# Performance work log

Hardware: AMD Instinct MI355X
Metric: run time of the kernel (lower is better)

The kernel has to match this reference:

```python
import jax, jax.numpy as jnp
import numpy as np
import math

SUB = 0.8  # subset fraction (init kwarg)


def _capsule_weighted_average(x):
    # x: [B, I, O, D, H, W]; norm-weighted average over input caps (dim 1)
    n = jnp.linalg.norm(x, axis=3, keepdims=True)  # [B, I, O, 1, H, W]
    return (n * x).sum(axis=1) / n.sum(axis=1)      # [B, O, D, H, W]


def setup_inputs() -> dict:
    key = jax.random.key(0)
    # [B, input_caps, output_caps, pose_dim, H, W, kh, kw]
    x = jax.random.normal(key, (8, 32, 32, 8, 14, 14, 3, 3), dtype=jnp.float32)
    return {"x": x}


def reference(x):
    B, I, O, D, H, W = x.shape[:6]
    x = x.reshape(B, I, O, D, H, W, -1)             # flatten kernel positions -> K
    # norm-weighted average over the K kernel positions
    xn = jnp.linalg.norm(x, axis=3, keepdims=True)  # [B, I, O, 1, H, W, K]
    x = (xn * x).sum(axis=-1) / xn.sum(axis=-1)     # [B, I, O, D, H, W]

    v = _capsule_weighted_average(x)                # [B, O, D, H, W]

    # 'mse' metric: negative dot product between consensus v and each input capsule
    losses = -(v[:, None] * x).sum(axis=3)          # [B, I, O, H, W]
    subset_size = math.ceil(SUB * I)
    # kthvalue (k-th smallest) along input-caps dim
    thr = jnp.sort(losses, axis=1)[:, subset_size - 1:subset_size]  # [B, 1, O, H, W]
    choose = (losses <= thr).astype(x.dtype)[:, :, :, None]          # [B, I, O, 1, H, W]
    x = x * jax.lax.stop_gradient(choose)

    return _capsule_weighted_average(x)             # [B, O, D, H, W]
```

## Files before the change

kernel.cpp:

```cpp
#include <hip/hip_runtime.h>

#define B 8
#define I 32
#define O 32
#define D 8
#define H 14
#define W 14
#define K 9
#define WK (W*K)
#define DSTRIDE (H*W*K)
#define OSTRIDE (D*H*W*K)
#define ISTRIDE (O*D*H*W*K)
#define BSTRIDE ((size_t)I*ISTRIDE)
#define SUBSET 26

__global__ __launch_bounds__(256) void caps_route_kernel(const float* __restrict__ x,
                                                         float* __restrict__ out) {
    const int bid = blockIdx.x;
    const int h = bid % H;
    const int o = (bid / H) % O;
    const int b = bid / (H * O);
    const int t = threadIdx.x;

    __shared__ float xs[2][D][WK];
    __shared__ float nk[2][WK];
    __shared__ float ys[I][D][W];
    __shared__ float ns[I][W];
    __shared__ float ls[I][W];
    __shared__ float vsh[D][W];
    __shared__ float thr[W];

    const float* xb = x + (size_t)b * BSTRIDE + (size_t)o * OSTRIDE + (size_t)h * WK;

    for (int i0 = 0; i0 < I; i0 += 2) {
        const float2* src0 = (const float2*)(xb + (size_t)(i0    ) * ISTRIDE);
        const float2* src1 = (const float2*)(xb + (size_t)(i0 + 1) * ISTRIDE);
        #pragma unroll
        for (int it = 0; it < 4; ++it) {
            int f = t + it * 256;
            if (f < 1008) {
                int ii = f / 504;
                int r  = f - ii * 504;
                int d  = r / 63;
                int j  = r - d * 63;
                const float2* src = ii ? src1 : src0;
                float2 v2 = src[d * (DSTRIDE/2) + j];
                xs[ii][d][2*j]   = v2.x;
                xs[ii][d][2*j+1] = v2.y;
            }
        }
        __syncthreads();

        if (t < 2 * WK) {
            int ii = t / WK, j = t - (t / WK) * WK;
            float s = 0.f;
            #pragma unroll
            for (int d = 0; d < D; ++d) { float v = xs[ii][d][j]; s += v * v; }
            nk[ii][j] = sqrtf(s);
        }
        __syncthreads();

        if (t < 2 * D * W) {
            int ii = t / (D * W);
            int r  = t - ii * (D * W);
            int d  = r / W, w = r - (r / W) * W;
            float num = 0.f, den = 0.f;
            #pragma unroll
            for (int k = 0; k < K; ++k) {
                float nv = nk[ii][w * K + k];
                num += nv * xs[ii][d][w * K + k];
                den += nv;
            }
            ys[i0 + ii][d][w] = num / den;
        }
        __syncthreads();
    }

    for (int f = t; f < I * W; f += 256) {
        int i = f / W, w = f - (f / W) * W;
        float s = 0.f;
        #pragma unroll
        for (int d = 0; d < D; ++d) { float v = ys[i][d][w]; s += v * v; }
        ns[i][w] = sqrtf(s);
    }
    __syncthreads();

    if (t < D * W) {
        int d = t / W, w = t - (t / W) * W;
        float num = 0.f, den = 0.f;
        #pragma unroll
        for (int i = 0; i < I; ++i) {
            float nv = ns[i][w];
            num += nv * ys[i][d][w];
            den += nv;
        }
        vsh[d][w] = num / den;
    }
    __syncthreads();

    for (int f = t; f < I * W; f += 256) {
        int i = f / W, w = f - (f / W) * W;
        float s = 0.f;
        #pragma unroll
        for (int d = 0; d < D; ++d) s += vsh[d][w] * ys[i][d][w];
        ls[i][w] = -s;
    }
    __syncthreads();

    for (int f = t; f < I * W; f += 256) {
        int i = f / W, w = f - (f / W) * W;
        float li = ls[i][w];
        int rank = 0;
        #pragma unroll
        for (int j = 0; j < I; ++j) {
            float lj = ls[j][w];
            rank += (lj < li || (lj == li && j < i)) ? 1 : 0;
        }
        if (rank == SUBSET - 1) thr[w] = li;
    }
    __syncthreads();

    if (t < D * W) {
        int d = t / W, w = t - (t / W) * W;
        float tw = thr[w];
        float num = 0.f, den = 0.f;
        #pragma unroll
        for (int i = 0; i < I; ++i) {
            float m  = (ls[i][w] <= tw) ? 1.f : 0.f;
            float nv = m * ns[i][w];
            num += nv * ys[i][d][w];
            den += nv;
        }
        out[(((size_t)b * O + o) * D + d) * (H * W) + h * W + w] = num / den;
    }
}

extern "C" void kernel_launch(void* const* d_in, const int* in_sizes, int n_in,
                              void* d_out, int out_size, void* d_ws, size_t ws_size,
                              hipStream_t stream) {
    const float* x = (const float*)d_in[0];
    float* out = (float*)d_out;
    dim3 grid(B * O * H);
    dim3 block(256);
    caps_route_kernel<<<grid, block, 0, stream>>>(x, out);
}
```

Measured before the change: 619.2 us.

## Assign one thread per input-capsule and width position with register-resident loads

Replaces the serial 16-iteration loop over input-capsule pairs, which had three block barriers per iteration, with 448 threads. Each thread loads its own 8x9 slab straight into registers and computes the kernel-position norm average locally. This removes the shared staging buffers and about 48 barriers, and exposes all 32 capsules' loads at once for more memory-level parallelism. The cost is per-thread loads of 9 contiguous floats at a stride of 36 bytes, which coalesce less well than the earlier float2 loads, plus higher register use per thread.

Result: faster. 605.8 us (-2.2%).

```diff
diff --git a/kernel.cpp b/kernel.cpp
--- a/kernel.cpp
+++ b/kernel.cpp
@@ -14,124 +14,102 @@
 #define BSTRIDE ((size_t)I*ISTRIDE)
 #define SUBSET 26
 
-__global__ __launch_bounds__(256) void caps_route_kernel(const float* __restrict__ x,
+__global__ __launch_bounds__(448) void caps_route_kernel(const float* __restrict__ x,
                                                          float* __restrict__ out) {
     const int bid = blockIdx.x;
     const int h = bid % H;
     const int o = (bid / H) % O;
     const int b = bid / (H * O);
     const int t = threadIdx.x;
+    const int i = t / W;
+    const int w = t - i * W;
 
-    __shared__ float xs[2][D][WK];
-    __shared__ float nk[2][WK];
     __shared__ float ys[I][D][W];
-    __shared__ float ns[I][W];
-    __shared__ float ls[I][W];
+    __shared__ float ns_s[I][W];
+    __shared__ float ls_s[I][W];
     __shared__ float vsh[D][W];
-    __shared__ float thr[W];
+    __shared__ float thr_s[W];
 
-    const float* xb = x + (size_t)b * BSTRIDE + (size_t)o * OSTRIDE + (size_t)h * WK;
+    const float* xp = x + (size_t)b * BSTRIDE + (size_t)i * ISTRIDE
+                        + (size_t)o * OSTRIDE + (size_t)h * WK + (size_t)w * K;
 
-    for (int i0 = 0; i0 < I; i0 += 2) {
-        const float2* src0 = (const float2*)(xb + (size_t)(i0    ) * ISTRIDE);
-        const float2* src1 = (const float2*)(xb + (size_t)(i0 + 1) * ISTRIDE);
+    float xv[D][K];
+    #pragma unroll
+    for (int d = 0; d < D; ++d) {
         #pragma unroll
-        for (int it = 0; it < 4; ++it) {
-            int f = t + it * 256;
-            if (f < 1008) {
-                int ii = f / 504;
-                int r  = f - ii * 504;
-                int d  = r / 63;
-                int j  = r - d * 63;
-                const float2* src = ii ? src1 : src0;
-                float2 v2 = src[d * (DSTRIDE/2) + j];
-                xs[ii][d][2*j]   = v2.x;
-                xs[ii][d][2*j+1] = v2.y;
-            }
+        for (int k = 0; k < K; ++k) {
+            xv[d][k] = xp[d * DSTRIDE + k];
         }
-        __syncthreads();
-
-        if (t < 2 * WK) {
-            int ii = t / WK, j = t - (t / WK) * WK;
-            float s = 0.f;
-            #pragma unroll
-            for (int d = 0; d < D; ++d) { float v = xs[ii][d][j]; s += v * v; }
-            nk[ii][j] = sqrtf(s);
-        }
-        __syncthreads();
-
-        if (t < 2 * D * W) {
-            int ii = t / (D * W);
-            int r  = t - ii * (D * W);
-            int d  = r / W, w = r - (r / W) * W;
-            float num = 0.f, den = 0.f;
-            #pragma unroll
-            for (int k = 0; k < K; ++k) {
-                float nv = nk[ii][w * K + k];
-                num += nv * xs[ii][d][w * K + k];
-                den += nv;
-            }
-            ys[i0 + ii][d][w] = num / den;
-        }
-        __syncthreads();
     }
 
-    for (int f = t; f < I * W; f += 256) {
-        int i = f / W, w = f - (f / W) * W;
+    float nk[K];
+    float den = 0.f;
+    #pragma unroll
+    for (int k = 0; k < K; ++k) {
         float s = 0.f;
         #pragma unroll
-        for (int d = 0; d < D; ++d) { float v = ys[i][d][w]; s += v * v; }
-        ns[i][w] = sqrtf(s);
+        for (int d = 0; d < D; ++d) { float v = xv[d][k]; s += v * v; }
+        nk[k] = sqrtf(s);
+        den += nk[k];
+    }
+    const float inv_den = 1.f / den;
+
+    float y[D];
+    float s2 = 0.f;
+    #pragma unroll
+    for (int d = 0; d < D; ++d) {
+        float num = 0.f;
+        #pragma unroll
+        for (int k = 0; k < K; ++k) num += nk[k] * xv[d][k];
+        y[d] = num * inv_den;
+        ys[i][d][w] = y[d];
+        s2 += y[d] * y[d];
+    }
+    const float nsv = sqrtf(s2);
+    ns_s[i][w] = nsv;
+    __syncthreads();
+
+    if (t < D * W) {
+        const int d = t / W, w2 = t - (t / W) * W;
+        float num = 0.f, dn = 0.f;
+        #pragma unroll
+        for (int j = 0; j < I; ++j) {
+            float nv = ns_s[j][w2];
+            num += nv * ys[j][d][w2];
+            dn += nv;
+        }
+        vsh[d][w2] = num / dn;
     }
     __syncthreads();
 
-    if (t < D * W) {
-        int d = t / W, w = t - (t / W) * W;
-        float num = 0.f, den = 0.f;
-        #pragma unroll
-        for (int i = 0; i < I; ++i) {
-            float nv = ns[i][w];
-            num += nv * ys[i][d][w];
-            den += nv;
-        }
-        vsh[d][w] = num / den;
-    }
+    float lv = 0.f;
+    #pragma unroll
+    for (int d = 0; d < D; ++d) lv += vsh[d][w] * y[d];
+    lv = -lv;
+    ls_s[i][w] = lv;
     __syncthreads();
 
-    for (int f = t; f < I * W; f += 256) {
-        int i = f / W, w = f - (f / W) * W;
-        float s = 0.f;
-        #pragma unroll
-        for (int d = 0; d < D; ++d) s += vsh[d][w] * ys[i][d][w];
-        ls[i][w] = -s;
+    int rank = 0;
+    #pragma unroll
+    for (int j = 0; j < I; ++j) {
+        float lj = ls_s[j][w];
+        rank += (lj < lv || (lj == lv && j < i)) ? 1 : 0;
     }
-    __syncthreads();
-
-    for (int f = t; f < I * W; f += 256) {
-        int i = f / W, w = f - (f / W) * W;
-        float li = ls[i][w];
-        int rank = 0;
-        #pragma unroll
-        for (int j = 0; j < I; ++j) {
-            float lj = ls[j][w];
-            rank += (lj < li || (lj == li && j < i)) ? 1 : 0;
-        }
-        if (rank == SUBSET - 1) thr[w] = li;
-    }
+    if (rank == SUBSET - 1) thr_s[w] = lv;
     __syncthreads();
 
     if (t < D * W) {
-        int d = t / W, w = t - (t / W) * W;
-        float tw = thr[w];
-        float num = 0.f, den = 0.f;
+        const int d = t / W, w2 = t - (t / W) * W;
+        const float tw = thr_s[w2];
+        float num = 0.f, dn = 0.f;
         #pragma unroll
-        for (int i = 0; i < I; ++i) {
-            float m  = (ls[i][w] <= tw) ? 1.f : 0.f;
-            float nv = m * ns[i][w];
-            num += nv * ys[i][d][w];
-            den += nv;
+        for (int j = 0; j < I; ++j) {
+            float m  = (ls_s[j][w2] <= tw) ? 1.f : 0.f;
+            float nv = m * ns_s[j][w2];
+            num += nv * ys[j][d][w2];
+            dn  += nv;
         }
-        out[(((size_t)b * O + o) * D + d) * (H * W) + h * W + w] = num / den;
+        out[(((size_t)b * O + o) * D + d) * (H * W) + h * W + w2] = num / dn;
     }
 }
 
@@ -141,6 +119,6 @@
     const float* x = (const float*)d_in[0];
     float* out = (float*)d_out;
     dim3 grid(B * O * H);
-    dim3 block(256);
+    dim3 block(I * W);
     caps_route_kernel<<<grid, block, 0, stream>>>(x, out);
 }
```
